# Kernel tuning notes

Measured on AMD Instinct MI355X. Metric: run time of the kernel, lower is better.

The kernel has to match this reference:

```python
import jax, jax.numpy as jnp
import numpy as np

B, S, D = 4, 256, 768      # batch, seq, activation_dim
F = 8192                   # dict_size (both modules)
K = 64                     # topk
C = 128                    # connections per downstream feature


def _topk_keep(post, k):
    """Keep top-k entries per row, zero elsewhere. post: [N, F]."""
    vals, idx = jax.lax.top_k(post, k)
    n = post.shape[0]
    return jnp.zeros_like(post).at[jnp.arange(n)[:, None], idx].set(vals)


def setup_inputs() -> dict:
    key = jax.random.key(0)
    ks = jax.random.split(key, 10)
    s = 1.0 / np.sqrt(D)
    return {
        "initial_acts": jax.random.normal(ks[0], (B, S, D), jnp.float32),
        "x_up": jax.random.normal(ks[1], (B, S, D), jnp.float32),
        "ln_scale": jax.random.uniform(ks[2], (B, S), jnp.float32, 0.5, 1.5),
        "W_enc_up": jax.random.normal(ks[3], (F, D), jnp.float32) * s,
        "b_enc_up": jnp.zeros((F,), jnp.float32),
        "W_dec_up": jax.random.normal(ks[4], (D, F), jnp.float32) * s,
        "b_dec_up": jax.random.normal(ks[5], (D,), jnp.float32) * 0.01,
        "W_enc_down": jax.random.normal(ks[6], (F, D), jnp.float32) * s,
        "b_enc_down": jnp.zeros((F,), jnp.float32),
        "W_dec_down": jax.random.normal(ks[7], (D, F), jnp.float32) * s,
        "b_dec_down": jax.random.normal(ks[8], (D,), jnp.float32) * 0.01,
        "conn": jax.random.randint(ks[9], (F, C), 0, F),  # all valid (no -1 pad)
    }


def reference(initial_acts, x_up, ln_scale,
              W_enc_up, b_enc_up, W_dec_up, b_dec_up,
              W_enc_down, b_enc_down, W_dec_down, b_dec_down,
              conn):
    b, s, d = initial_acts.shape
    n = b * s
    x0 = initial_acts.reshape(n, d)
    xu = x_up.reshape(n, d)
    ln = ln_scale.reshape(n)

    # --- vanilla_forward on upstream: TopK SAE encode + decode ---
    post_up = jax.nn.relu((xu - b_dec_up) @ W_enc_up.T + b_enc_up)  # [n, F]
    feat_up = _topk_keep(post_up, K)
    recon_up = feat_up @ W_dec_up.T + b_dec_up                      # [n, d]

    # --- pruned downstream path ---
    fd = W_enc_down.shape[0]
    fu = W_dec_up.shape[1]
    # virtual weights: down_encoder @ up_decoder  -> [F_down, F_up]
    virtual = W_enc_down @ W_dec_up
    # connection mask from index tensor [F_down, C]
    mask = jnp.zeros((fd, fu), bool).at[jnp.arange(fd)[:, None], conn].set(True)
    masked = jnp.where(mask, virtual, jnp.zeros((), virtual.dtype))

    approx = x0 @ W_enc_down.T                                      # initial contributions [n, F_down]
    approx = approx + feat_up @ masked.T + W_enc_down @ b_dec_up    # pruned contributions + b_dec term
    approx = approx / ln[:, None] + b_enc_down - W_enc_down @ b_dec_down

    feat_down = _topk_keep(approx, K)
    recon_down = feat_down @ W_dec_down.T + b_dec_down              # [n, d]

    return jnp.stack([recon_up.reshape(b, s, d), recon_down.reshape(b, s, d)])
```

## Files before the change

### kernel.cpp

```cpp
#include <hip/hip_runtime.h>


#define NTOK 1024
#define DIM  768
#define FF   8192
#define KK   64
#define CC   128
#define KSEL 96
#define CAP  128

typedef unsigned short u16;
typedef unsigned int   u32;
typedef __attribute__((ext_vector_type(8))) short short8;
typedef __attribute__((ext_vector_type(4))) float floatx4;

__device__ __forceinline__ float bits2f(u32 v) {
    float f; __builtin_memcpy(&f, &v, 4); return f;
}
__device__ __forceinline__ float bf2f(u16 u) { return bits2f(((u32)u) << 16); }
__device__ __forceinline__ u16 f2bf(float f) {
    u32 u; __builtin_memcpy(&u, &f, 4);
    u32 lsb = (u >> 16) & 1u;
    u += 0x7fffu + lsb;
    return (u16)(u >> 16);
}
__device__ __forceinline__ u32 f2key(float x) {
    u32 u; __builtin_memcpy(&u, &x, 4);
    return (u & 0x80000000u) ? ~u : (u | 0x80000000u);
}

__global__ __launch_bounds__(256) void convert_kernel(const float* __restrict__ src,
                                                      u16* __restrict__ dst, int n4) {
    int i = blockIdx.x * 256 + threadIdx.x;
    if (i < n4) {
        float4 v = ((const float4*)src)[i];
        ushort4 o;
        o.x = f2bf(v.x); o.y = f2bf(v.y); o.z = f2bf(v.z); o.w = f2bf(v.w);
        ((ushort4*)dst)[i] = o;
    }
}

__global__ __launch_bounds__(256) void transpose_kernel(const float* __restrict__ in,
                                                        float* __restrict__ out) {
    __shared__ float tile[32][33];
    int f0 = blockIdx.x * 32, d0 = blockIdx.y * 32;
    int tx = threadIdx.x, ty = threadIdx.y;
#pragma unroll
    for (int i = 0; i < 4; ++i)
        tile[ty + 8 * i][tx] = in[(size_t)(d0 + ty + 8 * i) * FF + f0 + tx];
    __syncthreads();
#pragma unroll
    for (int i = 0; i < 4; ++i)
        out[(size_t)(f0 + ty + 8 * i) * DIM + d0 + tx] = tile[tx][ty + 8 * i];
}

__global__ __launch_bounds__(64) void bias_kernel(const float* __restrict__ Weu,
                                                  const float* __restrict__ Wed,
                                                  const float* __restrict__ bdu,
                                                  const float* __restrict__ bdd,
                                                  float* __restrict__ sF,
                                                  float* __restrict__ tuF,
                                                  float* __restrict__ tdF,
                                                  double* __restrict__ s64,
                                                  double* __restrict__ tu64,
                                                  double* __restrict__ td64) {
    int f = blockIdx.x, lane = threadIdx.x;
    double su = 0.0, tu = 0.0, td = 0.0;
    for (int i = lane; i < DIM; i += 64) {
        double bu = (double)bdu[i], bd = (double)bdd[i];
        su += (double)Weu[(size_t)f * DIM + i] * bu;
        double w = (double)Wed[(size_t)f * DIM + i];
        tu += w * bu;
        td += w * bd;
    }
#pragma unroll
    for (int off = 32; off; off >>= 1) {
        su += __shfl_xor(su, off);
        tu += __shfl_xor(tu, off);
        td += __shfl_xor(td, off);
    }
    if (lane == 0) {
        sF[f] = (float)su; tuF[f] = (float)tu; tdF[f] = (float)td;
        s64[f] = su; tu64[f] = tu; td64[f] = td;
    }
}

template <int MODE>
__global__ __launch_bounds__(256) void gemm_mfma(const u16* __restrict__ A16,
                                                 const u16* __restrict__ B16,
                                                 u16* __restrict__ Xout,
                                                 const float* __restrict__ sF,
                                                 const float* __restrict__ b_enc) {
    __shared__ __align__(16) u16 As[128 * 40];
    __shared__ __align__(16) u16 Bs[128 * 40];
    int tid = threadIdx.x;
    int wave = tid >> 6, lane = tid & 63;
    int lm = lane & 15, quad = lane >> 4;
    int m0 = blockIdx.y * 128, n0 = blockIdx.x * 128;
    int wm = (wave >> 1) * 64, wn = (wave & 1) * 64;
    floatx4 acc[4][4];
#pragma unroll
    for (int i = 0; i < 4; ++i)
#pragma unroll
        for (int j = 0; j < 4; ++j)
            acc[i][j] = (floatx4){0.f, 0.f, 0.f, 0.f};
    int r = tid >> 2;
    int s = (tid & 3) * 8;
    const u16* gA = A16 + (size_t)(m0 + r) * DIM + s;
    const u16* gB = B16 + (size_t)(n0 + r) * DIM + s;
    for (int k0 = 0; k0 < DIM; k0 += 32) {
        __syncthreads();
        *(int4*)&As[r * 40 + s]          = *(const int4*)(gA + k0);
        *(int4*)&As[(r + 64) * 40 + s]   = *(const int4*)(gA + (size_t)64 * DIM + k0);
        *(int4*)&Bs[r * 40 + s]          = *(const int4*)(gB + k0);
        *(int4*)&Bs[(r + 64) * 40 + s]   = *(const int4*)(gB + (size_t)64 * DIM + k0);
        __syncthreads();
        short8 af[4], bfr[4];
#pragma unroll
        for (int mi = 0; mi < 4; ++mi)
            af[mi] = *(const short8*)&As[(wm + mi * 16 + lm) * 40 + quad * 8];
#pragma unroll
        for (int ni = 0; ni < 4; ++ni)
            bfr[ni] = *(const short8*)&Bs[(wn + ni * 16 + lm) * 40 + quad * 8];
#pragma unroll
        for (int mi = 0; mi < 4; ++mi)
#pragma unroll
            for (int ni = 0; ni < 4; ++ni)
                acc[mi][ni] = __builtin_amdgcn_mfma_f32_16x16x32_bf16(
                    af[mi], bfr[ni], acc[mi][ni], 0, 0, 0);
    }
#pragma unroll
    for (int ni = 0; ni < 4; ++ni) {
        int col = n0 + wn + ni * 16 + lm;
        float sub = 0.f, bb = 0.f;
        if (MODE == 0) { sub = sF[col]; bb = b_enc[col]; }
#pragma unroll
        for (int mi = 0; mi < 4; ++mi) {
#pragma unroll
            for (int reg = 0; reg < 4; ++reg) {
                int row = m0 + wm + mi * 16 + quad * 4 + reg;
                float v = acc[mi][ni][reg];
                if (MODE == 0) { v = v - sub + bb; v = v > 0.f ? v : 0.f; }
                Xout[(size_t)row * FF + col] = f2bf(v);
            }
        }
    }
}

__global__ __launch_bounds__(256) void select_kernel(const u16* __restrict__ X16,
                                                     u16* __restrict__ cand,
                                                     int* __restrict__ cnt) {
    __shared__ u32 hist[256];
    __shared__ u32 sh_prefix;
    __shared__ int sh_k;
    __shared__ u32 sh_cntG, sh_cntE;
    __shared__ int eqidx[256];
    const int rrow = blockIdx.x, tid = threadIdx.x;
    const u16* xr = X16 + (size_t)rrow * FF;
    if (tid == 0) { sh_prefix = 0; sh_k = KSEL; }
    __syncthreads();
    for (int pass = 0; pass < 4; ++pass) {
        hist[tid] = 0;
        __syncthreads();
        u32 prefix = sh_prefix;
        int shift = 24 - 8 * pass;
        for (int i = tid; i < FF; i += 256) {
            u32 key = f2key(bf2f(xr[i]));
            if (pass == 0 || (key >> (shift + 8)) == prefix)
                atomicAdd(&hist[(key >> shift) & 255u], 1u);
        }
        __syncthreads();
        if (tid == 0) {
            int rem = sh_k;
            int b = 255;
            for (; b > 0; --b) {
                int h = (int)hist[b];
                if (rem <= h) break;
                rem -= h;
            }
            sh_prefix = (prefix << 8) | (u32)b;
            sh_k = rem;
        }
        __syncthreads();
    }
    u32 T = sh_prefix;
    if (tid == 0) { sh_cntG = 0; sh_cntE = 0; }
    __syncthreads();
    u16* cr = cand + (size_t)rrow * CAP;
    for (int i = tid; i < FF; i += 256) {
        u32 key = f2key(bf2f(xr[i]));
        if (key > T) {
            u32 p = atomicAdd(&sh_cntG, 1u);
            if (p < CAP) cr[p] = (u16)i;
        } else if (key == T) {
            u32 p = atomicAdd(&sh_cntE, 1u);
            if (p < 256) eqidx[p] = i;
        }
    }
    __syncthreads();
    if (tid == 0) {
        int G = (int)sh_cntG; if (G > CAP) G = CAP;
        int ne = (int)sh_cntE; if (ne > 256) ne = 256;
        int total = G;
        for (int q = 0; q < ne && total < CAP; ++q) cr[total++] = (u16)eqidx[q];
        cnt[rrow] = total;
    }
}

__device__ __forceinline__ bool sort_before(double av, int ai, double bv, int bi) {
    return (av > bv) || (av == bv && ai < bi);
}
__device__ void bitonic128(double* sv, int* si, int tid) {
    for (int k = 2; k <= 128; k <<= 1) {
        for (int j = k >> 1; j > 0; j >>= 1) {
            __syncthreads();
            if (tid < 64) {
                int i = ((tid & ~(j - 1)) << 1) | (tid & (j - 1));
                int l = i, rr = i + j;
                bool bfirst = sort_before(sv[rr], si[rr], sv[l], si[l]);
                bool doswap = ((i & k) == 0) ? bfirst : !bfirst;
                if (doswap) {
                    double tv = sv[l]; sv[l] = sv[rr]; sv[rr] = tv;
                    int ti = si[l]; si[l] = si[rr]; si[rr] = ti;
                }
            }
        }
    }
    __syncthreads();
}

__global__ __launch_bounds__(256) void fixup_up(const float* __restrict__ xu,
                                                const float* __restrict__ Weu,
                                                const double* __restrict__ s64,
                                                const float* __restrict__ beu,
                                                const u16* __restrict__ cand,
                                                const int* __restrict__ cnt,
                                                float* __restrict__ vals,
                                                int* __restrict__ idxs) {
    __shared__ float xrow[DIM];
    __shared__ double sv[128];
    __shared__ int si[128];
    int t = blockIdx.x, tid = threadIdx.x, wave = tid >> 6, lane = tid & 63;
    for (int i = tid; i < DIM; i += 256) xrow[i] = xu[(size_t)t * DIM + i];
    for (int c = tid; c < 128; c += 256) { sv[c] = -1.0e300; si[c] = 0x7fffffff; }
    __syncthreads();
    int nc = cnt[t]; if (nc > 128) nc = 128;
    for (int c = wave; c < nc; c += 4) {
        int f = (int)cand[(size_t)t * CAP + c];
        const float* wr = Weu + (size_t)f * DIM;
        double p = 0.0;
#pragma unroll
        for (int i = 0; i < 12; ++i) {
            int d = lane + 64 * i;
            p += (double)xrow[d] * (double)wr[d];
        }
#pragma unroll
        for (int off = 32; off; off >>= 1) p += __shfl_xor(p, off);
        if (lane == 0) {
            double v = p - s64[f] + (double)beu[f];
            v = v > 0.0 ? v : 0.0;
            sv[c] = v; si[c] = f;
        }
    }
    __syncthreads();
    bitonic128(sv, si, tid);
    if (tid < KK) {
        vals[(size_t)t * KK + tid] = (float)sv[tid];
        idxs[(size_t)t * KK + tid] = si[tid];
    }
}

__global__ __launch_bounds__(256) void fixup_dn(const float* __restrict__ x0,
                                                const float* __restrict__ Wed,
                                                const float* __restrict__ WduT,
                                                const double* __restrict__ tu64,
                                                const double* __restrict__ td64,
                                                const float* __restrict__ bed,
                                                const float* __restrict__ ln,
                                                const u16* __restrict__ cclean,
                                                const float* __restrict__ vals_up,
                                                const int* __restrict__ idx_up,
                                                const u16* __restrict__ cand,
                                                const int* __restrict__ cnt,
                                                float* __restrict__ vals,
                                                int* __restrict__ idxs) {
    __shared__ float xrow[DIM];
    __shared__ u32 bm[256];
    __shared__ int fl[KK];
    __shared__ float zl[KK];
    __shared__ double sv[128];
    __shared__ int si[128];
    int t = blockIdx.x, tid = threadIdx.x, wave = tid >> 6, lane = tid & 63;
    for (int i = tid; i < DIM; i += 256) xrow[i] = x0[(size_t)t * DIM + i];
    if (tid < 256) bm[tid] = 0;
    for (int c = tid; c < 128; c += 256) { sv[c] = -1.0e300; si[c] = 0x7fffffff; }
    __syncthreads();
    if (tid < KK) {
        int f = idx_up[(size_t)t * KK + tid];
        fl[tid] = f; zl[tid] = vals_up[(size_t)t * KK + tid];
        atomicOr(&bm[f >> 5], 1u << (f & 31));
    }
    __syncthreads();
    int nc = cnt[t]; if (nc > 128) nc = 128;
    double lnt = (double)ln[t];
    for (int c = wave; c < nc; c += 4) {
        int f = (int)cand[(size_t)t * CAP + c];
        const float* wr = Wed + (size_t)f * DIM;
        double p = 0.0;
#pragma unroll
        for (int i = 0; i < 12; ++i) {
            int d = lane + 64 * i;
            p += (double)xrow[d] * (double)wr[d];
        }
        const u16* crow = cclean + (size_t)f * CC;
        int e0 = (int)crow[lane], e1 = (int)crow[lane + 64];
        bool h0 = (e0 != 0xFFFF) && ((bm[e0 >> 5] >> (e0 & 31)) & 1u);
        bool h1 = (e1 != 0xFFFF) && ((bm[e1 >> 5] >> (e1 & 31)) & 1u);
        unsigned long long m0 = __ballot(h0), m1 = __ballot(h1);
        while (m0 | m1) {
            int fu;
            if (m0) {
                int b = __ffsll((long long)m0) - 1; m0 &= m0 - 1;
                fu = __shfl(e0, b);
            } else {
                int b = __ffsll((long long)m1) - 1; m1 &= m1 - 1;
                fu = __shfl(e1, b);
            }
            unsigned long long zm = __ballot(fl[lane & 63] == fu && lane < KK);
            float z = zl[__ffsll((long long)zm) - 1];
            const float* du = WduT + (size_t)fu * DIM;
            double vp = 0.0;
#pragma unroll
            for (int i = 0; i < 12; ++i) {
                int d = lane + 64 * i;
                vp += (double)wr[d] * (double)du[d];
            }
            p += (double)z * vp;
        }
#pragma unroll
        for (int off = 32; off; off >>= 1) p += __shfl_xor(p, off);
        if (lane == 0) {
            double v = (p + tu64[f]) / lnt + (double)bed[f] - td64[f];
            sv[c] = v; si[c] = f;
        }
    }
    __syncthreads();
    bitonic128(sv, si, tid);
    if (tid < KK) {
        vals[(size_t)t * KK + tid] = (float)sv[tid];
        idxs[(size_t)t * KK + tid] = si[tid];
    }
}

__global__ __launch_bounds__(128) void dedup_deg_kernel(const int* __restrict__ conn,
                                                        u32* __restrict__ deg) {
    __shared__ int row[CC];
    int fd = blockIdx.x, c = threadIdx.x;
    int v = conn[(size_t)fd * CC + c];
    row[c] = v;
    __syncthreads();
    bool dup = false;
    for (int j = 0; j < c; ++j) dup |= (row[j] == v);
    if (!dup) atomicAdd(&deg[v], 1u);
}

__global__ __launch_bounds__(256) void scan_kernel(const u32* __restrict__ deg,
                                                   u32* __restrict__ offs) {
    __shared__ u32 sdeg[FF];
    __shared__ u32 part[256];
    int tid = threadIdx.x;
    for (int i = tid; i < FF; i += 256) sdeg[i] = deg[i];
    __syncthreads();
    u32 s = 0;
    for (int j = 0; j < 32; ++j) s += sdeg[tid * 32 + j];
    part[tid] = s;
    __syncthreads();
    if (tid == 0) {
        u32 run = 0;
        for (int i = 0; i < 256; ++i) { u32 v = part[i]; part[i] = run; run += v; }
        offs[FF] = run;
    }
    __syncthreads();
    u32 run = part[tid];
    for (int j = 0; j < 32; ++j) { offs[tid * 32 + j] = run; run += sdeg[tid * 32 + j]; }
}

__global__ __launch_bounds__(128) void fill_kernel(const int* __restrict__ conn,
                                                   const u32* __restrict__ offs,
                                                   u32* __restrict__ cursor,
                                                   u16* __restrict__ inv_fd,
                                                   u16* __restrict__ cclean) {
    __shared__ int row[CC];
    int fd = blockIdx.x, c = threadIdx.x;
    int v = conn[(size_t)fd * CC + c];
    row[c] = v;
    __syncthreads();
    bool dup = false;
    for (int j = 0; j < c; ++j) dup |= (row[j] == v);
    cclean[(size_t)fd * CC + c] = dup ? (u16)0xFFFF : (u16)v;
    if (!dup) {
        u32 slot = atomicAdd(&cursor[v], 1u);
        inv_fd[offs[v] + slot] = (u16)fd;
    }
}

__global__ __launch_bounds__(256) void vconn_kernel(const u16* __restrict__ Wed16,
                                                    const float* __restrict__ WduT,
                                                    const u32* __restrict__ offs,
                                                    const u16* __restrict__ inv_fd,
                                                    u16* __restrict__ v_inv16) {
    __shared__ float row[DIM];
    int fu = blockIdx.x;
    for (int i = threadIdx.x; i < DIM; i += 256) row[i] = WduT[(size_t)fu * DIM + i];
    __syncthreads();
    u32 s = offs[fu], e = offs[fu + 1];
    int wave = threadIdx.x >> 6, lane = threadIdx.x & 63;
    const float4* row4 = (const float4*)row;
    for (u32 p = s + wave; p < e; p += 4) {
        int fd = (int)inv_fd[p];
        const ushort4* wr = (const ushort4*)(Wed16 + (size_t)fd * DIM);
        float acc = 0.f;
#pragma unroll
        for (int i = 0; i < 3; ++i) {
            ushort4 u = wr[lane + 64 * i];
            float4 rv = row4[lane + 64 * i];
            acc = fmaf(bf2f(u.x), rv.x, acc);
            acc = fmaf(bf2f(u.y), rv.y, acc);
            acc = fmaf(bf2f(u.z), rv.z, acc);
            acc = fmaf(bf2f(u.w), rv.w, acc);
        }
#pragma unroll
        for (int off = 32; off; off >>= 1) acc += __shfl_xor(acc, off);
        if (lane == 0) v_inv16[p] = f2bf(acc);
    }
}

__global__ __launch_bounds__(256) void phase2_kernel(u16* __restrict__ X16,
                                                     const float* __restrict__ vals_up,
                                                     const int* __restrict__ idx_up,
                                                     const u32* __restrict__ offs,
                                                     const u16* __restrict__ inv_fd,
                                                     const u16* __restrict__ v_inv16,
                                                     const float* __restrict__ tuF,
                                                     const float* __restrict__ tdF,
                                                     const float* __restrict__ bed,
                                                     const float* __restrict__ ln) {
    __shared__ float acc[FF];
    __shared__ float z[KK];
    __shared__ int fidx[KK];
    int t = blockIdx.x, tid = threadIdx.x;
    for (int i = tid; i < FF; i += 256) acc[i] = 0.f;
    if (tid < KK) { z[tid] = vals_up[(size_t)t * KK + tid]; fidx[tid] = idx_up[(size_t)t * KK + tid]; }
    __syncthreads();
    for (int j = 0; j < KK; ++j) {
        float zj = z[j];
        int f = fidx[j];
        u32 s = offs[f], e = offs[f + 1];
        for (u32 p = s + tid; p < e; p += 256)
            atomicAdd(&acc[(int)inv_fd[p]], zj * bf2f(v_inv16[p]));
    }
    __syncthreads();
    float lnv = ln[t];
    for (int i = tid; i < FF; i += 256) {
        float v = bf2f(X16[(size_t)t * FF + i]) + acc[i] + tuF[i];
        v = v / lnv + bed[i] - tdF[i];
        X16[(size_t)t * FF + i] = f2bf(v);
    }
}

__global__ __launch_bounds__(256) void decode_kernel(const float* __restrict__ vals,
                                                     const int* __restrict__ idxs,
                                                     const float* __restrict__ WdT,
                                                     const float* __restrict__ b_dec,
                                                     float* __restrict__ outp) {
    __shared__ float z[KK];
    __shared__ int fidx[KK];
    int t = blockIdx.x, tid = threadIdx.x;
    if (tid < KK) { z[tid] = vals[(size_t)t * KK + tid]; fidx[tid] = idxs[(size_t)t * KK + tid]; }
    __syncthreads();
    float a0 = 0.f, a1 = 0.f, a2 = 0.f;
    for (int j = 0; j < KK; ++j) {
        const float* wr = WdT + (size_t)fidx[j] * DIM;
        float zj = z[j];
        a0 = fmaf(zj, wr[tid], a0);
        a1 = fmaf(zj, wr[tid + 256], a1);
        a2 = fmaf(zj, wr[tid + 512], a2);
    }
    outp[(size_t)t * DIM + tid]       = a0 + b_dec[tid];
    outp[(size_t)t * DIM + tid + 256] = a1 + b_dec[tid + 256];
    outp[(size_t)t * DIM + tid + 512] = a2 + b_dec[tid + 512];
}

extern "C" void kernel_launch(void* const* d_in, const int* in_sizes, int n_in,
                              void* d_out, int out_size, void* d_ws, size_t ws_size,
                              hipStream_t stream) {
    const float* x0  = (const float*)d_in[0];
    const float* xu  = (const float*)d_in[1];
    const float* ln  = (const float*)d_in[2];
    const float* Weu = (const float*)d_in[3];
    const float* beu = (const float*)d_in[4];
    const float* Wdu = (const float*)d_in[5];
    const float* bdu = (const float*)d_in[6];
    const float* Wed = (const float*)d_in[7];
    const float* bed = (const float*)d_in[8];
    const float* Wdd = (const float*)d_in[9];
    const float* bdd = (const float*)d_in[10];
    const int* conn = (const int*)d_in[11];
    float* out = (float*)d_out;

    char* w = (char*)d_ws;
    size_t off = 0;
    auto take = [&](size_t bytes) { char* p = w + off; off = (off + bytes + 255) & ~(size_t)255; return p; };
    u16*   X16     = (u16*)take((size_t)NTOK * FF * 2);
    u16*   B16     = (u16*)take((size_t)FF * DIM * 2);
    float* WddT    = (float*)X16;
    float* WduT    = (float*)take((size_t)FF * DIM * 4);
    u16*   A16u    = (u16*)take((size_t)NTOK * DIM * 2);
    u16*   A16d    = (u16*)take((size_t)NTOK * DIM * 2);
    u16*   v_inv16 = (u16*)take((size_t)FF * CC * 2);
    u16*   inv_fd  = (u16*)take((size_t)FF * CC * 2);
    u16*   cclean  = (u16*)take((size_t)FF * CC * 2);
    u16*   cand_u  = (u16*)take((size_t)NTOK * CAP * 2);
    u16*   cand_d  = (u16*)take((size_t)NTOK * CAP * 2);
    int*   cnt_u   = (int*)take(NTOK * 4);
    int*   cnt_d   = (int*)take(NTOK * 4);
    float* vals_up = (float*)take((size_t)NTOK * KK * 4);
    int*   idx_up  = (int*)take((size_t)NTOK * KK * 4);
    float* vals_dn = (float*)take((size_t)NTOK * KK * 4);
    int*   idx_dn  = (int*)take((size_t)NTOK * KK * 4);
    float* sF      = (float*)take(FF * 4);
    float* tuF     = (float*)take(FF * 4);
    float* tdF     = (float*)take(FF * 4);
    double* s64    = (double*)take(FF * 8);
    double* tu64   = (double*)take(FF * 8);
    double* td64   = (double*)take(FF * 8);
    u32*   deg     = (u32*)take(FF * 4);
    u32*   cursor  = (u32*)take(FF * 4);
    u32*   offs    = (u32*)take((FF + 8) * 4);

    dim3 tgrid(FF / 32, DIM / 32), tblk(32, 8);
    dim3 ggrid(FF / 128, NTOK / 128);

    transpose_kernel<<<tgrid, tblk, 0, stream>>>(Wdu, WduT);
    bias_kernel<<<FF, 64, 0, stream>>>(Weu, Wed, bdu, bdd, sF, tuF, tdF, s64, tu64, td64);
    hipMemsetAsync(deg, 0, 2 * FF * sizeof(u32), stream);
    dedup_deg_kernel<<<FF, CC, 0, stream>>>(conn, deg);
    scan_kernel<<<1, 256, 0, stream>>>(deg, offs);
    fill_kernel<<<FF, CC, 0, stream>>>(conn, offs, cursor, inv_fd, cclean);

    int nA4 = NTOK * DIM / 4, nB4 = FF * DIM / 4;
    convert_kernel<<<(nA4 + 255) / 256, 256, 0, stream>>>(xu, A16u, nA4);
    convert_kernel<<<(nA4 + 255) / 256, 256, 0, stream>>>(x0, A16d, nA4);
    convert_kernel<<<(nB4 + 255) / 256, 256, 0, stream>>>(Weu, B16, nB4);

    gemm_mfma<0><<<ggrid, 256, 0, stream>>>(A16u, B16, X16, sF, beu);
    select_kernel<<<NTOK, 256, 0, stream>>>(X16, cand_u, cnt_u);
    fixup_up<<<NTOK, 256, 0, stream>>>(xu, Weu, s64, beu, cand_u, cnt_u, vals_up, idx_up);

    convert_kernel<<<(nB4 + 255) / 256, 256, 0, stream>>>(Wed, B16, nB4);
    gemm_mfma<1><<<ggrid, 256, 0, stream>>>(A16d, B16, X16, sF, beu);
    vconn_kernel<<<FF, 256, 0, stream>>>(B16, WduT, offs, inv_fd, v_inv16);
    phase2_kernel<<<NTOK, 256, 0, stream>>>(X16, vals_up, idx_up, offs, inv_fd, v_inv16,
                                            tuF, tdF, bed, ln);
    select_kernel<<<NTOK, 256, 0, stream>>>(X16, cand_d, cnt_d);
    fixup_dn<<<NTOK, 256, 0, stream>>>(x0, Wed, WduT, tu64, td64, bed, ln, cclean,
                                       vals_up, idx_up, cand_d, cnt_d, vals_dn, idx_dn);

    decode_kernel<<<NTOK, 256, 0, stream>>>(vals_up, idx_up, WduT, bdu, out);
    transpose_kernel<<<tgrid, tblk, 0, stream>>>(Wdd, WddT);
    decode_kernel<<<NTOK, 256, 0, stream>>>(vals_dn, idx_dn, WddT, bdd,
                                            out + (size_t)NTOK * DIM);
}
```

Baseline: 863.8 us.

## Fuse downstream select into phase2, chunk vconn, stage select rows in LDS

```diff
diff --git a/kernel.cpp b/kernel.cpp
--- a/kernel.cpp
+++ b/kernel.cpp
@@ -6,7 +6,8 @@
 #define FF   8192
 #define KK   64
 #define CC   128
-#define KSEL 96
+#define KSEL_UP 80
+#define KSEL_DN 96
 #define CAP  128
 
 typedef unsigned short u16;
@@ -147,17 +148,25 @@
     }
 }
 
-__global__ __launch_bounds__(256) void select_kernel(const u16* __restrict__ X16,
-                                                     u16* __restrict__ cand,
-                                                     int* __restrict__ cnt) {
+__global__ __launch_bounds__(256) void select_up_kernel(const u16* __restrict__ X16,
+                                                        u16* __restrict__ cand,
+                                                        int* __restrict__ cnt) {
+    __shared__ float xr[FF];
     __shared__ u32 hist[256];
     __shared__ u32 sh_prefix;
     __shared__ int sh_k;
     __shared__ u32 sh_cntG, sh_cntE;
     __shared__ int eqidx[256];
     const int rrow = blockIdx.x, tid = threadIdx.x;
-    const u16* xr = X16 + (size_t)rrow * FF;
-    if (tid == 0) { sh_prefix = 0; sh_k = KSEL; }
+    const ushort4* src = (const ushort4*)(X16 + (size_t)rrow * FF);
+    for (int i = tid; i < FF / 4; i += 256) {
+        ushort4 u = src[i];
+        xr[i * 4]     = bf2f(u.x);
+        xr[i * 4 + 1] = bf2f(u.y);
+        xr[i * 4 + 2] = bf2f(u.z);
+        xr[i * 4 + 3] = bf2f(u.w);
+    }
+    if (tid == 0) { sh_prefix = 0; sh_k = KSEL_UP; }
     __syncthreads();
     for (int pass = 0; pass < 4; ++pass) {
         hist[tid] = 0;
@@ -165,7 +174,7 @@
         u32 prefix = sh_prefix;
         int shift = 24 - 8 * pass;
         for (int i = tid; i < FF; i += 256) {
-            u32 key = f2key(bf2f(xr[i]));
+            u32 key = f2key(xr[i]);
             if (pass == 0 || (key >> (shift + 8)) == prefix)
                 atomicAdd(&hist[(key >> shift) & 255u], 1u);
         }
@@ -188,7 +197,7 @@
     __syncthreads();
     u16* cr = cand + (size_t)rrow * CAP;
     for (int i = tid; i < FF; i += 256) {
-        u32 key = f2key(bf2f(xr[i]));
+        u32 key = f2key(xr[i]);
         if (key > T) {
             u32 p = atomicAdd(&sh_cntG, 1u);
             if (p < CAP) cr[p] = (u16)i;
@@ -404,53 +413,65 @@
     }
 }
 
-__global__ __launch_bounds__(256) void vconn_kernel(const u16* __restrict__ Wed16,
-                                                    const float* __restrict__ WduT,
-                                                    const u32* __restrict__ offs,
-                                                    const u16* __restrict__ inv_fd,
-                                                    u16* __restrict__ v_inv16) {
-    __shared__ float row[DIM];
-    int fu = blockIdx.x;
-    for (int i = threadIdx.x; i < DIM; i += 256) row[i] = WduT[(size_t)fu * DIM + i];
+__global__ __launch_bounds__(256) void vconn_chunk(const u16* __restrict__ Wed16,
+                                                   const float* __restrict__ WduT,
+                                                   const u32* __restrict__ offs,
+                                                   const u16* __restrict__ inv_fd,
+                                                   u16* __restrict__ v_inv16,
+                                                   int chunk, int first) {
+    __shared__ float row[192];
+    int fu = blockIdx.x, tid = threadIdx.x;
+    if (tid < 192) row[tid] = WduT[(size_t)fu * DIM + chunk * 192 + tid];
     __syncthreads();
     u32 s = offs[fu], e = offs[fu + 1];
-    int wave = threadIdx.x >> 6, lane = threadIdx.x & 63;
-    const float4* row4 = (const float4*)row;
-    for (u32 p = s + wave; p < e; p += 4) {
-        int fd = (int)inv_fd[p];
-        const ushort4* wr = (const ushort4*)(Wed16 + (size_t)fd * DIM);
-        float acc = 0.f;
-#pragma unroll
-        for (int i = 0; i < 3; ++i) {
-            ushort4 u = wr[lane + 64 * i];
-            float4 rv = row4[lane + 64 * i];
-            acc = fmaf(bf2f(u.x), rv.x, acc);
-            acc = fmaf(bf2f(u.y), rv.y, acc);
-            acc = fmaf(bf2f(u.z), rv.z, acc);
-            acc = fmaf(bf2f(u.w), rv.w, acc);
-        }
-#pragma unroll
-        for (int off = 32; off; off >>= 1) acc += __shfl_xor(acc, off);
-        if (lane == 0) v_inv16[p] = f2bf(acc);
-    }
-}
-
-__global__ __launch_bounds__(256) void phase2_kernel(u16* __restrict__ X16,
-                                                     const float* __restrict__ vals_up,
-                                                     const int* __restrict__ idx_up,
-                                                     const u32* __restrict__ offs,
-                                                     const u16* __restrict__ inv_fd,
-                                                     const u16* __restrict__ v_inv16,
-                                                     const float* __restrict__ tuF,
-                                                     const float* __restrict__ tdF,
-                                                     const float* __restrict__ bed,
-                                                     const float* __restrict__ ln) {
+    int wave = tid >> 6, lane = tid & 63;
+    int sub = lane >> 4, sl = lane & 15;
+    for (u32 p0 = s + (u32)wave * 4; p0 < e; p0 += 16) {
+        u32 p = p0 + (u32)sub;
+        bool valid = p < e;
+        float a = 0.f;
+        if (valid) {
+            int fd = (int)inv_fd[p];
+            const u16* wr = Wed16 + (size_t)fd * DIM + chunk * 192;
+#pragma unroll
+            for (int i = 0; i < 12; ++i)
+                a = fmaf(bf2f(wr[sl + 16 * i]), row[sl + 16 * i], a);
+        }
+        a += __shfl_xor(a, 1);
+        a += __shfl_xor(a, 2);
+        a += __shfl_xor(a, 4);
+        a += __shfl_xor(a, 8);
+        if (valid && sl == 0) {
+            if (first) v_inv16[p] = f2bf(a);
+            else       v_inv16[p] = f2bf(bf2f(v_inv16[p]) + a);
+        }
+    }
+}
+
+__global__ __launch_bounds__(256) void phase2sel(const u16* __restrict__ X16,
+                                                 const float* __restrict__ vals_up,
+                                                 const int* __restrict__ idx_up,
+                                                 const u32* __restrict__ offs,
+                                                 const u16* __restrict__ inv_fd,
+                                                 const u16* __restrict__ v_inv16,
+                                                 const float* __restrict__ tuF,
+                                                 const float* __restrict__ tdF,
+                                                 const float* __restrict__ bed,
+                                                 const float* __restrict__ ln,
+                                                 u16* __restrict__ cand,
+                                                 int* __restrict__ cnt) {
     __shared__ float acc[FF];
     __shared__ float z[KK];
     __shared__ int fidx[KK];
+    __shared__ u32 hist[256];
+    __shared__ u32 sh_prefix;
+    __shared__ int sh_k;
+    __shared__ u32 sh_cntG, sh_cntE;
+    __shared__ int eqidx[256];
     int t = blockIdx.x, tid = threadIdx.x;
     for (int i = tid; i < FF; i += 256) acc[i] = 0.f;
     if (tid < KK) { z[tid] = vals_up[(size_t)t * KK + tid]; fidx[tid] = idx_up[(size_t)t * KK + tid]; }
+    if (tid == 0) { sh_prefix = 0; sh_k = KSEL_DN; }
     __syncthreads();
     for (int j = 0; j < KK; ++j) {
         float zj = z[j];
@@ -461,10 +482,63 @@
     }
     __syncthreads();
     float lnv = ln[t];
+    const ushort4* xsrc = (const ushort4*)(X16 + (size_t)t * FF);
+    for (int i = tid; i < FF / 4; i += 256) {
+        ushort4 u = xsrc[i];
+#pragma unroll
+        for (int q = 0; q < 4; ++q) {
+            int idx = i * 4 + q;
+            float xv = bf2f(q == 0 ? u.x : q == 1 ? u.y : q == 2 ? u.z : u.w);
+            float v = xv + acc[idx] + tuF[idx];
+            acc[idx] = v / lnv + bed[idx] - tdF[idx];
+        }
+    }
+    __syncthreads();
+    for (int pass = 0; pass < 4; ++pass) {
+        hist[tid] = 0;
+        __syncthreads();
+        u32 prefix = sh_prefix;
+        int shift = 24 - 8 * pass;
+        for (int i = tid; i < FF; i += 256) {
+            u32 key = f2key(acc[i]);
+            if (pass == 0 || (key >> (shift + 8)) == prefix)
+                atomicAdd(&hist[(key >> shift) & 255u], 1u);
+        }
+        __syncthreads();
+        if (tid == 0) {
+            int rem = sh_k;
+            int b = 255;
+            for (; b > 0; --b) {
+                int h = (int)hist[b];
+                if (rem <= h) break;
+                rem -= h;
+            }
+            sh_prefix = (prefix << 8) | (u32)b;
+            sh_k = rem;
+        }
+        __syncthreads();
+    }
+    u32 T = sh_prefix;
+    if (tid == 0) { sh_cntG = 0; sh_cntE = 0; }
+    __syncthreads();
+    u16* cr = cand + (size_t)t * CAP;
     for (int i = tid; i < FF; i += 256) {
-        float v = bf2f(X16[(size_t)t * FF + i]) + acc[i] + tuF[i];
-        v = v / lnv + bed[i] - tdF[i];
-        X16[(size_t)t * FF + i] = f2bf(v);
+        u32 key = f2key(acc[i]);
+        if (key > T) {
+            u32 p = atomicAdd(&sh_cntG, 1u);
+            if (p < CAP) cr[p] = (u16)i;
+        } else if (key == T) {
+            u32 p = atomicAdd(&sh_cntE, 1u);
+            if (p < 256) eqidx[p] = i;
+        }
+    }
+    __syncthreads();
+    if (tid == 0) {
+        int G = (int)sh_cntG; if (G > CAP) G = CAP;
+        int ne = (int)sh_cntE; if (ne > 256) ne = 256;
+        int total = G;
+        for (int q = 0; q < ne && total < CAP; ++q) cr[total++] = (u16)eqidx[q];
+        cnt[t] = total;
     }
 }
 
@@ -515,8 +589,7 @@
     u16*   B16     = (u16*)take((size_t)FF * DIM * 2);
     float* WddT    = (float*)X16;
     float* WduT    = (float*)take((size_t)FF * DIM * 4);
-    u16*   A16u    = (u16*)take((size_t)NTOK * DIM * 2);
-    u16*   A16d    = (u16*)take((size_t)NTOK * DIM * 2);
+    u16*   A16     = (u16*)take((size_t)NTOK * DIM * 2);
     u16*   v_inv16 = (u16*)take((size_t)FF * CC * 2);
     u16*   inv_fd  = (u16*)take((size_t)FF * CC * 2);
     u16*   cclean  = (u16*)take((size_t)FF * CC * 2);
@@ -540,6 +613,7 @@
 
     dim3 tgrid(FF / 32, DIM / 32), tblk(32, 8);
     dim3 ggrid(FF / 128, NTOK / 128);
+    int nA4 = NTOK * DIM / 4, nB4 = FF * DIM / 4;
 
     transpose_kernel<<<tgrid, tblk, 0, stream>>>(Wdu, WduT);
     bias_kernel<<<FF, 64, 0, stream>>>(Weu, Wed, bdu, bdd, sF, tuF, tdF, s64, tu64, td64);
@@ -548,21 +622,21 @@
     scan_kernel<<<1, 256, 0, stream>>>(deg, offs);
     fill_kernel<<<FF, CC, 0, stream>>>(conn, offs, cursor, inv_fd, cclean);
 
-    int nA4 = NTOK * DIM / 4, nB4 = FF * DIM / 4;
-    convert_kernel<<<(nA4 + 255) / 256, 256, 0, stream>>>(xu, A16u, nA4);
-    convert_kernel<<<(nA4 + 255) / 256, 256, 0, stream>>>(x0, A16d, nA4);
+    convert_kernel<<<(nA4 + 255) / 256, 256, 0, stream>>>(xu, A16, nA4);
     convert_kernel<<<(nB4 + 255) / 256, 256, 0, stream>>>(Weu, B16, nB4);
-
-    gemm_mfma<0><<<ggrid, 256, 0, stream>>>(A16u, B16, X16, sF, beu);
-    select_kernel<<<NTOK, 256, 0, stream>>>(X16, cand_u, cnt_u);
+    gemm_mfma<0><<<ggrid, 256, 0, stream>>>(A16, B16, X16, sF, beu);
+    select_up_kernel<<<NTOK, 256, 0, stream>>>(X16, cand_u, cnt_u);
     fixup_up<<<NTOK, 256, 0, stream>>>(xu, Weu, s64, beu, cand_u, cnt_u, vals_up, idx_up);
 
+    convert_kernel<<<(nA4 + 255) / 256, 256, 0, stream>>>(x0, A16, nA4);
     convert_kernel<<<(nB4 + 255) / 256, 256, 0, stream>>>(Wed, B16, nB4);
-    gemm_mfma<1><<<ggrid, 256, 0, stream>>>(A16d, B16, X16, sF, beu);
-    vconn_kernel<<<FF, 256, 0, stream>>>(B16, WduT, offs, inv_fd, v_inv16);
-    phase2_kernel<<<NTOK, 256, 0, stream>>>(X16, vals_up, idx_up, offs, inv_fd, v_inv16,
-                                            tuF, tdF, bed, ln);
-    select_kernel<<<NTOK, 256, 0, stream>>>(X16, cand_d, cnt_d);
+    gemm_mfma<1><<<ggrid, 256, 0, stream>>>(A16, B16, X16, sF, beu);
+    vconn_chunk<<<FF, 256, 0, stream>>>(B16, WduT, offs, inv_fd, v_inv16, 0, 1);
+    vconn_chunk<<<FF, 256, 0, stream>>>(B16, WduT, offs, inv_fd, v_inv16, 1, 0);
+    vconn_chunk<<<FF, 256, 0, stream>>>(B16, WduT, offs, inv_fd, v_inv16, 2, 0);
+    vconn_chunk<<<FF, 256, 0, stream>>>(B16, WduT, offs, inv_fd, v_inv16, 3, 0);
+    phase2sel<<<NTOK, 256, 0, stream>>>(X16, vals_up, idx_up, offs, inv_fd, v_inv16,
+                                        tuF, tdF, bed, ln, cand_d, cnt_d);
     fixup_dn<<<NTOK, 256, 0, stream>>>(x0, Wed, WduT, tu64, td64, bed, ln, cclean,
                                        vals_up, idx_up, cand_d, cnt_d, vals_dn, idx_dn);
 
```

After: 856.0 us. About the same (-0.9%).
